# Optimization experiments

Measured on AMD Instinct MI355X. Metric: run time of the kernel, lower is better.

## Reference

```python
import jax, jax.numpy as jnp
import numpy as np

EPS_IN = 1e-5   # InstanceNorm1d eps
EPS_DM = 1e-8   # demodulation eps


def _dcoef(weight, style):
    # rsqrt(sum_i (W[o,i]*s[b,i])^2 + eps) -> [B, out]
    return jax.lax.rsqrt(jnp.einsum('oi,bi->bo', jnp.square(weight), jnp.square(style)) + EPS_DM)


def setup_inputs() -> dict:
    key = jax.random.key(0)
    ks = jax.random.split(key, 7)
    B, S, H = 8, 1024, 1024
    lim = 1.0 / np.sqrt(H)
    u = lambda k, shp: jax.random.uniform(k, shp, jnp.float32, -lim, lim)
    return {
        'x': jax.random.normal(ks[0], (B, S, H), jnp.float32),
        'q_weight': u(ks[1], (H, H)),
        'k_weight': u(ks[2], (H, H)),
        'v_weight': u(ks[3], (H, H)),
        'w_weight': u(ks[4], (H, H)),
        'u_weight': u(ks[5], (H, H)),
        'styles': jax.random.normal(ks[6], (B, 2 * H), jnp.float32) * 0.5 + 1.0,
        'num_heads': 16,
    }


def reference(x, q_weight, k_weight, v_weight, w_weight, u_weight, styles, num_heads):
    B, S, H = x.shape
    nh = num_heads
    d = H // nh
    scale = jnp.asarray(d, x.dtype) ** -0.5

    s1 = styles[:, :H]   # modulates input hidden dim of q/k/v
    s2 = styles[:, H:]   # modulates input hidden dim of w/u and v output

    # per-sample modulation + InstanceNorm over hidden dim
    x = x * s1[:, None, :]
    mu = jnp.mean(x, axis=-1, keepdims=True)
    var = jnp.mean(jnp.square(x - mu), axis=-1, keepdims=True)
    x = (x - mu) * jax.lax.rsqrt(var + EPS_IN)

    q_dc = _dcoef(q_weight, s1)  # [B,H]
    k_dc = _dcoef(k_weight, s1)
    v_dc = _dcoef(v_weight, s1)
    w_dc = _dcoef(w_weight, s2)
    u_dc = _dcoef(u_weight, s2)

    def heads(t):  # [B,S,H] -> [B,nh,S,d]
        return t.reshape(B, S, nh, d).transpose(0, 2, 1, 3)

    q = heads(jnp.einsum('bsh,oh->bso', x, q_weight) * q_dc[:, None, :])
    k = heads(jnp.einsum('bsh,oh->bso', x, k_weight) * k_dc[:, None, :])
    v_flat = jnp.einsum('bsh,oh->bso', x, v_weight) * v_dc[:, None, :] * s2[:, None, :]
    skip = v_flat
    v = heads(v_flat)

    attn = jnp.einsum('bhqd,bhkd->bhqk', q, k) * scale
    attn = jax.nn.softmax(attn, axis=-1)
    out = jnp.einsum('bhqk,bhkd->bhqd', attn, v).transpose(0, 2, 1, 3).reshape(B, S, H)

    out = jnp.einsum('bsh,oh->bso', out, w_weight) * w_dc[:, None, :]
    skip = jnp.einsum('bsh,oh->bso', skip, u_weight) * u_dc[:, None, :]
    return out + skip
```

## Files before the change

kernel.cpp:

```cpp
#include <hip/hip_runtime.h>
#include <hip/hip_bf16.h>

#define B_ 8
#define S_ 1024
#define H_ 1024
#define NH 16
#define DH 64
#define BS (B_*S_)
#define L2E 1.44269504f

typedef unsigned short u16;
typedef __attribute__((ext_vector_type(8))) short bf16x8;
typedef __attribute__((ext_vector_type(4))) float f32x4;
typedef __attribute__((ext_vector_type(4))) u16 u16x4;

#define MFMA(a,b,c) __builtin_amdgcn_mfma_f32_16x16x32_bf16((a),(b),(c),0,0,0)

__device__ __forceinline__ u16 f2bf(float f) {
  union { float f; unsigned u; } v; v.f = f;
  unsigned r = v.u + 0x7fffu + ((v.u >> 16) & 1u);
  return (u16)(r >> 16);
}

__device__ __forceinline__ unsigned packbf2(float a, float b) {
  union { __hip_bfloat162 h; unsigned u; } v;
  v.h = __float22bfloat162_rn(float2{a, b});
  return v.u;
}

__device__ __forceinline__ void gload16(const u16* g, u16* l) {
  __builtin_amdgcn_global_load_lds(
      (const __attribute__((address_space(1))) unsigned int*)g,
      (__attribute__((address_space(3))) unsigned int*)l, 16, 0, 0);
}

__global__ __launch_bounds__(256) void dcoef_kernel(
    const float* __restrict__ qw, const float* __restrict__ kw,
    const float* __restrict__ vw, const float* __restrict__ ww,
    const float* __restrict__ uw, const float* __restrict__ styles,
    float* __restrict__ dc) {
  int bi = blockIdx.x;
  int wsel = bi >> 10;
  int o = bi & 1023;
  const float* W = (wsel == 0) ? qw : (wsel == 1) ? kw : (wsel == 2) ? vw
                   : (wsel == 3) ? ww : uw;
  int soff = (wsel < 3) ? 0 : H_;
  int tid = threadIdx.x;
  float4 w4 = *(const float4*)(W + (size_t)o * H_ + tid * 4);
  float w2x = w4.x * w4.x, w2y = w4.y * w4.y, w2z = w4.z * w4.z, w2w = w4.w * w4.w;
  float acc[8];
#pragma unroll
  for (int b = 0; b < 8; b++) {
    float4 s4 = *(const float4*)(styles + (size_t)b * 2 * H_ + soff + tid * 4);
    acc[b] = w2x * s4.x * s4.x + w2y * s4.y * s4.y + w2z * s4.z * s4.z + w2w * s4.w * s4.w;
  }
#pragma unroll
  for (int off = 1; off < 64; off <<= 1)
#pragma unroll
    for (int b = 0; b < 8; b++) acc[b] += __shfl_xor(acc[b], off);
  __shared__ float red[4][8];
  int w = tid >> 6, l = tid & 63;
  if (l == 0)
#pragma unroll
    for (int b = 0; b < 8; b++) red[w][b] = acc[b];
  __syncthreads();
  if (tid < 8) {
    int b = tid;
    float v = red[0][b] + red[1][b] + red[2][b] + red[3][b];
    float r = rsqrtf(v + 1e-8f);
    if (wsel == 2) r *= styles[(size_t)b * 2 * H_ + H_ + o];
    dc[(size_t)wsel * B_ * H_ + b * H_ + o] = r;
  }
}

__global__ __launch_bounds__(256) void wconv_kernel(
    const float* __restrict__ qw, const float* __restrict__ kw,
    const float* __restrict__ vw, const float* __restrict__ ww,
    const float* __restrict__ uw, u16* __restrict__ w16) {
  int i = blockIdx.x * 256 + threadIdx.x;
  int idx = i * 4;
  int wsel = idx >> 20;
  int off = idx & (H_ * H_ - 1);
  const float* W = (wsel == 0) ? qw : (wsel == 1) ? kw : (wsel == 2) ? vw
                   : (wsel == 3) ? ww : uw;
  float4 v = *(const float4*)(W + off);
  u16x4 o = { f2bf(v.x), f2bf(v.y), f2bf(v.z), f2bf(v.w) };
  *(u16x4*)(w16 + idx) = o;
}

__global__ __launch_bounds__(256) void ln_kernel(
    const float* __restrict__ x, const float* __restrict__ styles,
    u16* __restrict__ xn) {
  int row = blockIdx.x;
  int b = row >> 10;
  int tid = threadIdx.x;
  const float4 xv = *(const float4*)(x + (size_t)row * H_ + tid * 4);
  const float4 sv = *(const float4*)(styles + (size_t)b * 2 * H_ + tid * 4);
  float v0 = xv.x * sv.x, v1 = xv.y * sv.y, v2 = xv.z * sv.z, v3 = xv.w * sv.w;
  float sum = v0 + v1 + v2 + v3;
  float sq = v0 * v0 + v1 * v1 + v2 * v2 + v3 * v3;
#pragma unroll
  for (int off = 1; off < 64; off <<= 1) {
    sum += __shfl_xor(sum, off);
    sq += __shfl_xor(sq, off);
  }
  __shared__ float rsum[4], rsq[4];
  int w = tid >> 6;
  if ((tid & 63) == 0) { rsum[w] = sum; rsq[w] = sq; }
  __syncthreads();
  sum = rsum[0] + rsum[1] + rsum[2] + rsum[3];
  sq = rsq[0] + rsq[1] + rsq[2] + rsq[3];
  float mean = sum * (1.f / H_);
  float var = sq * (1.f / H_) - mean * mean;
  float rstd = rsqrtf(var + 1e-5f);
  u16x4 o = { f2bf((v0 - mean) * rstd), f2bf((v1 - mean) * rstd),
              f2bf((v2 - mean) * rstd), f2bf((v3 - mean) * rstd) };
  *(u16x4*)(xn + (size_t)row * H_ + tid * 4) = o;
}

__device__ __forceinline__ void gemm128_core(
    const u16* __restrict__ Arow, const u16* __restrict__ Brow, int K,
    u16* ldsA, u16* ldsB, f32x4 acc[4][4]) {
  const int tid = threadIdx.x;
  const int l = tid & 63, w = tid >> 6;
  const int wm = (w >> 1) * 64, wn = (w & 1) * 64;
  const int lrow = l & 15, lko = (l >> 4) * 8;
  const int srow = tid >> 2;
  const int scol = (tid & 3) * 8;
  for (int k0 = 0; k0 < K; k0 += 32) {
    __syncthreads();
    gload16(Arow + (size_t)srow * K + k0 + scol,        ldsA + srow * 32 + scol);
    gload16(Arow + (size_t)(srow + 64) * K + k0 + scol, ldsA + (srow + 64) * 32 + scol);
    gload16(Brow + (size_t)srow * K + k0 + scol,        ldsB + srow * 32 + scol);
    gload16(Brow + (size_t)(srow + 64) * K + k0 + scol, ldsB + (srow + 64) * 32 + scol);
    __syncthreads();
    bf16x8 af[4], bfr[4];
#pragma unroll
    for (int i = 0; i < 4; i++)
      af[i] = *(const bf16x8*)&ldsA[(wm + i * 16 + lrow) * 32 + lko];
#pragma unroll
    for (int i = 0; i < 4; i++)
      bfr[i] = *(const bf16x8*)&ldsB[(wn + i * 16 + lrow) * 32 + lko];
#pragma unroll
    for (int mi = 0; mi < 4; mi++)
#pragma unroll
      for (int ni = 0; ni < 4; ni++)
        acc[mi][ni] = MFMA(af[mi], bfr[ni], acc[mi][ni]);
  }
}

__global__ __launch_bounds__(256) void qkv_kernel(
    const u16* __restrict__ xn, const u16* __restrict__ w16,
    const float* __restrict__ dc, u16* __restrict__ Qb, u16* __restrict__ Kb,
    u16* __restrict__ VT, u16* __restrict__ vfl) {
  __shared__ u16 ldsA[128 * 32], ldsB[128 * 32];
  int bm = blockIdx.x;
  int bn = blockIdx.y;
  f32x4 acc[4][4] = {};
  gemm128_core(xn + (size_t)bm * 128 * H_, w16 + (size_t)bn * 128 * H_, H_,
               ldsA, ldsB, acc);
  int l = threadIdx.x & 63, w = threadIdx.x >> 6;
  int wm = (w >> 1) * 64, wn = (w & 1) * 64;
  int wsel = bn >> 3;
  int col0 = (bn & 7) * 128 + wn;
  int row0 = bm * 128 + wm;
  const float* dcw = dc + (size_t)wsel * B_ * H_;
  float extra = (wsel == 0) ? 0.125f * L2E : 1.0f;
#pragma unroll
  for (int mi = 0; mi < 4; mi++) {
#pragma unroll
    for (int ni = 0; ni < 4; ni++) {
      int col = col0 + ni * 16 + (l & 15);
      int hh = col >> 6, dd = col & 63;
      int s_base = (row0 + mi * 16 + (l >> 4) * 4) & 1023;
      int b = (row0 + mi * 16 + (l >> 4) * 4) >> 10;
      float dcv = dcw[b * H_ + col] * extra;
      u16 bv[4];
#pragma unroll
      for (int rr = 0; rr < 4; rr++)
        bv[rr] = f2bf(acc[mi][ni][rr] * dcv);
      if (wsel == 0) {
#pragma unroll
        for (int rr = 0; rr < 4; rr++)
          Qb[((size_t)(b * NH + hh) * S_ + s_base + rr) * DH + dd] = bv[rr];
      } else if (wsel == 1) {
#pragma unroll
        for (int rr = 0; rr < 4; rr++)
          Kb[((size_t)(b * NH + hh) * S_ + s_base + rr) * DH + dd] = bv[rr];
      } else {
        u16x4 pv = { bv[0], bv[1], bv[2], bv[3] };
        *(u16x4*)&VT[((size_t)(b * NH + hh) * DH + dd) * S_ + s_base] = pv;
#pragma unroll
        for (int rr = 0; rr < 4; rr++)
          vfl[(size_t)(row0 + mi * 16 + (l >> 4) * 4 + rr) * H_ + col] = bv[rr];
      }
    }
  }
}

__global__ __launch_bounds__(512) void attn_kernel(
    const u16* __restrict__ Qb, const u16* __restrict__ Kb,
    const u16* __restrict__ VT, u16* __restrict__ xat) {
  __shared__ u16 ldsK[2][64 * 64];
  __shared__ u16 ldsV[2][64 * 64];
  __shared__ unsigned pls_all[8][16 * 36];
  int tid = threadIdx.x;
  int l = tid & 63, w = tid >> 6;
  int qblk = blockIdx.x;
  int h = blockIdx.y;
  int b = blockIdx.z;
  int q0 = qblk * 256 + w * 32;
  const u16* Qp = Qb + ((size_t)(b * NH + h) * S_ + q0) * DH;
  const u16* Kp = Kb + (size_t)(b * NH + h) * S_ * DH;
  const u16* Vp = VT + (size_t)(b * NH + h) * DH * S_;
  unsigned* pls = pls_all[w];
  int lr = l & 15, lg = l >> 4;
  int sw = (lr & 7) << 3;
  bf16x8 qfA0 = *(const bf16x8*)(Qp + lr * 64 + lg * 8);
  bf16x8 qfA1 = *(const bf16x8*)(Qp + lr * 64 + 32 + lg * 8);
  bf16x8 qfB0 = *(const bf16x8*)(Qp + (16 + lr) * 64 + lg * 8);
  bf16x8 qfB1 = *(const bf16x8*)(Qp + (16 + lr) * 64 + 32 + lg * 8);
  int srow = tid >> 3, schunk = tid & 7;
  int ssw = (schunk * 8) ^ ((srow & 7) << 3);
  const u16* Ksrc = Kp + (size_t)srow * DH + ssw;
  const u16* Vsrc = Vp + (size_t)srow * S_ + ssw;
  u16* Kdst = &ldsK[0][srow * 64 + schunk * 8];
  u16* Vdst = &ldsV[0][srow * 64 + schunk * 8];
  gload16(Ksrc, Kdst);
  gload16(Vsrc, Vdst);
  f32x4 accA[4] = {}, accB[4] = {};
  float mA = -1e30f, lsA = 0.f, mB = -1e30f, lsB = 0.f;
  asm volatile("s_waitcnt vmcnt(0)" ::: "memory");
  __builtin_amdgcn_s_barrier();
  int cur = 0;
  for (int t = 0; t < 16; ++t) {
    if (t < 15) {
      gload16(Ksrc + (size_t)(t + 1) * 64 * DH, Kdst + (cur ^ 1) * 64 * 64);
      gload16(Vsrc + (size_t)(t + 1) * 64,      Vdst + (cur ^ 1) * 64 * 64);
    }
    const u16* Kt = &ldsK[cur][0];
    const u16* Vt = &ldsV[cur][0];
#pragma unroll
    for (int g = 0; g < 2; g++) {
      bf16x8 q0f = (g == 0) ? qfA0 : qfB0;
      bf16x8 q1f = (g == 0) ? qfA1 : qfB1;
      float mreg = (g == 0) ? mA : mB;
      float lsreg = (g == 0) ? lsA : lsB;
      f32x4 st[4];
#pragma unroll
      for (int nt = 0; nt < 4; nt++) {
        bf16x8 kf0 = *(const bf16x8*)&Kt[(nt * 16 + lr) * 64 + ((lg * 8) ^ sw)];
        bf16x8 kf1 = *(const bf16x8*)&Kt[(nt * 16 + lr) * 64 + ((32 + lg * 8) ^ sw)];
        f32x4 z = {0.f, 0.f, 0.f, 0.f};
        z = MFMA(kf0, q0f, z);
        z = MFMA(kf1, q1f, z);
        st[nt] = z;
      }
      float tm = st[0][0];
#pragma unroll
      for (int nt = 0; nt < 4; nt++)
#pragma unroll
        for (int rr = 0; rr < 4; rr++) tm = fmaxf(tm, st[nt][rr]);
      tm = fmaxf(tm, __shfl_xor(tm, 16));
      tm = fmaxf(tm, __shfl_xor(tm, 32));
      float mn = fmaxf(mreg, tm);
      float al = __builtin_exp2f(mreg - mn);
      float rs = 0.f;
#pragma unroll
      for (int nt = 0; nt < 4; nt++)
#pragma unroll
        for (int rr = 0; rr < 4; rr++) {
          st[nt][rr] = __builtin_exp2f(st[nt][rr] - mn);
          rs += st[nt][rr];
        }
      rs += __shfl_xor(rs, 16);
      rs += __shfl_xor(rs, 32);
      if (g == 0) { mA = mn; lsA = lsA * al + rs; }
      else        { mB = mn; lsB = lsB * al + rs; }
      {
        unsigned* base = pls + lr * 36;
#pragma unroll
        for (int nt = 0; nt < 4; nt++) {
          uint2 pw = { packbf2(st[nt][0], st[nt][1]),
                       packbf2(st[nt][2], st[nt][3]) };
          *(uint2*)&base[nt * 8 + lg * 2] = pw;
        }
      }
      bf16x8 pb0 = *(const bf16x8*)&pls[lr * 36 + lg * 4];
      bf16x8 pb1 = *(const bf16x8*)&pls[lr * 36 + 16 + lg * 4];
#pragma unroll
      for (int nt = 0; nt < 4; nt++) {
        bf16x8 vf0 = *(const bf16x8*)&Vt[(nt * 16 + lr) * 64 + ((lg * 8) ^ sw)];
        bf16x8 vf1 = *(const bf16x8*)&Vt[(nt * 16 + lr) * 64 + ((32 + lg * 8) ^ sw)];
        if (g == 0) {
          accA[nt][0] *= al; accA[nt][1] *= al; accA[nt][2] *= al; accA[nt][3] *= al;
          accA[nt] = MFMA(vf0, pb0, accA[nt]);
          accA[nt] = MFMA(vf1, pb1, accA[nt]);
        } else {
          accB[nt][0] *= al; accB[nt][1] *= al; accB[nt][2] *= al; accB[nt][3] *= al;
          accB[nt] = MFMA(vf0, pb0, accB[nt]);
          accB[nt] = MFMA(vf1, pb1, accB[nt]);
        }
      }
    }
    asm volatile("s_waitcnt vmcnt(0)" ::: "memory");
    __builtin_amdgcn_s_barrier();
    cur ^= 1;
  }
  float invA = 1.f / lsA, invB = 1.f / lsB;
#pragma unroll
  for (int nt = 0; nt < 4; nt++) {
    u16x4 oA = { f2bf(accA[nt][0] * invA), f2bf(accA[nt][1] * invA),
                 f2bf(accA[nt][2] * invA), f2bf(accA[nt][3] * invA) };
    *(u16x4*)(xat + ((size_t)(b * S_) + q0 + lr) * H_ + h * DH + nt * 16 + lg * 4) = oA;
    u16x4 oB = { f2bf(accB[nt][0] * invB), f2bf(accB[nt][1] * invB),
                 f2bf(accB[nt][2] * invB), f2bf(accB[nt][3] * invB) };
    *(u16x4*)(xat + ((size_t)(b * S_) + q0 + 16 + lr) * H_ + h * DH + nt * 16 + lg * 4) = oB;
  }
}

__global__ __launch_bounds__(256) void out_kernel(
    const u16* __restrict__ xat, const u16* __restrict__ vfl,
    const u16* __restrict__ w16, const float* __restrict__ dc,
    float* __restrict__ out) {
  __shared__ u16 ldsA[128 * 32], ldsB[128 * 32];
  int bm = blockIdx.x;
  int bn = blockIdx.y;
  f32x4 acc[4][4] = {};
  gemm128_core(xat + (size_t)bm * 128 * H_,
               w16 + (size_t)3 * H_ * H_ + (size_t)bn * 128 * H_, H_,
               ldsA, ldsB, acc);
  int l = threadIdx.x & 63, w = threadIdx.x >> 6;
  int wm = (w >> 1) * 64, wn = (w & 1) * 64;
  int col0 = bn * 128 + wn;
  int row0 = bm * 128 + wm;
  int b = row0 >> 10;
  const float* wdc = dc + (size_t)3 * B_ * H_ + b * H_;
  const float* udc = dc + (size_t)4 * B_ * H_ + b * H_;
  float ratio[4], ud[4];
#pragma unroll
  for (int ni = 0; ni < 4; ni++) {
    int col = col0 + ni * 16 + (l & 15);
    ud[ni] = udc[col];
    ratio[ni] = wdc[col] / ud[ni];
  }
#pragma unroll
  for (int mi = 0; mi < 4; mi++)
#pragma unroll
    for (int ni = 0; ni < 4; ni++)
#pragma unroll
      for (int rr = 0; rr < 4; rr++) acc[mi][ni][rr] *= ratio[ni];
  gemm128_core(vfl + (size_t)bm * 128 * H_,
               w16 + (size_t)4 * H_ * H_ + (size_t)bn * 128 * H_, H_,
               ldsA, ldsB, acc);
#pragma unroll
  for (int mi = 0; mi < 4; mi++)
#pragma unroll
    for (int ni = 0; ni < 4; ni++) {
      int col = col0 + ni * 16 + (l & 15);
#pragma unroll
      for (int rr = 0; rr < 4; rr++) {
        int row = row0 + mi * 16 + (l >> 4) * 4 + rr;
        out[(size_t)row * H_ + col] = acc[mi][ni][rr] * ud[ni];
      }
    }
}

extern "C" void kernel_launch(void* const* d_in, const int* in_sizes, int n_in,
                              void* d_out, int out_size, void* d_ws, size_t ws_size,
                              hipStream_t stream) {
  const float* x = (const float*)d_in[0];
  const float* qw = (const float*)d_in[1];
  const float* kw = (const float*)d_in[2];
  const float* vw = (const float*)d_in[3];
  const float* ww = (const float*)d_in[4];
  const float* uw = (const float*)d_in[5];
  const float* styles = (const float*)d_in[6];
  float* out = (float*)d_out;

  char* ws = (char*)d_ws;
  size_t need = 163840 + (size_t)5 * H_ * H_ * 2 + (size_t)6 * BS * H_ * 2;
  if (ws_size < need) return;
  float* dc = (float*)ws;
  u16* w16 = (u16*)(ws + 163840);
  u16* xn  = w16 + (size_t)5 * H_ * H_;
  u16* Qb  = xn + (size_t)BS * H_;
  u16* Kb  = Qb + (size_t)BS * H_;
  u16* VT  = Kb + (size_t)BS * H_;
  u16* vfl = VT + (size_t)BS * H_;
  u16* xat = vfl + (size_t)BS * H_;

  dcoef_kernel<<<dim3(5 * H_), dim3(256), 0, stream>>>(qw, kw, vw, ww, uw, styles, dc);
  wconv_kernel<<<dim3(5120), dim3(256), 0, stream>>>(qw, kw, vw, ww, uw, w16);
  ln_kernel<<<dim3(BS), dim3(256), 0, stream>>>(x, styles, xn);
  qkv_kernel<<<dim3(64, 24), dim3(256), 0, stream>>>(xn, w16, dc, Qb, Kb, VT, vfl);
  attn_kernel<<<dim3(4, NH, B_), dim3(512), 0, stream>>>(Qb, Kb, VT, xat);
  out_kernel<<<dim3(64, 8), dim3(256), 0, stream>>>(xat, vfl, w16, dc, out);
}
```

Baseline: 228.7 us.

## Triple-buffer attention K/V loads, add lazy softmax rescale, setprio, and remap blocks

The attention kernel moves from double-buffered to triple-buffered K/V tiles in LDS, prefetching two tiles ahead and waiting with vmcnt(2) so global loads overlap more compute. Online-softmax rescaling is skipped when the new tile max stays within a threshold of the running max (a lazy-rescale trick that stays exact). MFMA sections are wrapped in s_setprio, and the grid is flattened with an index remap that spreads heads and batches across XCDs for better L2 locality. The extra LDS buffer may reduce occupancy.

```diff
diff --git a/kernel.cpp b/kernel.cpp
--- a/kernel.cpp
+++ b/kernel.cpp
@@ -201,14 +201,16 @@
 __global__ __launch_bounds__(512) void attn_kernel(
     const u16* __restrict__ Qb, const u16* __restrict__ Kb,
     const u16* __restrict__ VT, u16* __restrict__ xat) {
-  __shared__ u16 ldsK[2][64 * 64];
-  __shared__ u16 ldsV[2][64 * 64];
+  __shared__ u16 ldsK[3][64 * 64];
+  __shared__ u16 ldsV[3][64 * 64];
   __shared__ unsigned pls_all[8][16 * 36];
   int tid = threadIdx.x;
   int l = tid & 63, w = tid >> 6;
-  int qblk = blockIdx.x;
-  int h = blockIdx.y;
-  int b = blockIdx.z;
+  int id = blockIdx.x;
+  int r = id & 7, rest = id >> 3;
+  int qblk = rest & 3, a = rest >> 2;
+  int hl = a * 8 + r;
+  int h = hl & 15, b = hl >> 4;
   int q0 = qblk * 256 + w * 32;
   const u16* Qp = Qb + ((size_t)(b * NH + h) * S_ + q0) * DH;
   const u16* Kp = Kb + (size_t)(b * NH + h) * S_ * DH;
@@ -216,27 +218,29 @@
   unsigned* pls = pls_all[w];
   int lr = l & 15, lg = l >> 4;
   int sw = (lr & 7) << 3;
+  int srow = tid >> 3, schunk = tid & 7;
+  int ssw = (schunk * 8) ^ ((srow & 7) << 3);
+  const u16* Ksrc = Kp + (size_t)srow * DH + ssw;
+  const u16* Vsrc = Vp + (size_t)srow * S_ + ssw;
+  int sdst = srow * 64 + schunk * 8;
+  gload16(Ksrc, &ldsK[0][sdst]);
+  gload16(Vsrc, &ldsV[0][sdst]);
+  gload16(Ksrc + 64 * DH, &ldsK[1][sdst]);
+  gload16(Vsrc + 64,      &ldsV[1][sdst]);
   bf16x8 qfA0 = *(const bf16x8*)(Qp + lr * 64 + lg * 8);
   bf16x8 qfA1 = *(const bf16x8*)(Qp + lr * 64 + 32 + lg * 8);
   bf16x8 qfB0 = *(const bf16x8*)(Qp + (16 + lr) * 64 + lg * 8);
   bf16x8 qfB1 = *(const bf16x8*)(Qp + (16 + lr) * 64 + 32 + lg * 8);
-  int srow = tid >> 3, schunk = tid & 7;
-  int ssw = (schunk * 8) ^ ((srow & 7) << 3);
-  const u16* Ksrc = Kp + (size_t)srow * DH + ssw;
-  const u16* Vsrc = Vp + (size_t)srow * S_ + ssw;
-  u16* Kdst = &ldsK[0][srow * 64 + schunk * 8];
-  u16* Vdst = &ldsV[0][srow * 64 + schunk * 8];
-  gload16(Ksrc, Kdst);
-  gload16(Vsrc, Vdst);
   f32x4 accA[4] = {}, accB[4] = {};
   float mA = -1e30f, lsA = 0.f, mB = -1e30f, lsB = 0.f;
-  asm volatile("s_waitcnt vmcnt(0)" ::: "memory");
+  asm volatile("s_waitcnt vmcnt(2)" ::: "memory");
   __builtin_amdgcn_s_barrier();
   int cur = 0;
   for (int t = 0; t < 16; ++t) {
-    if (t < 15) {
-      gload16(Ksrc + (size_t)(t + 1) * 64 * DH, Kdst + (cur ^ 1) * 64 * 64);
-      gload16(Vsrc + (size_t)(t + 1) * 64,      Vdst + (cur ^ 1) * 64 * 64);
+    if (t + 2 < 16) {
+      int nb = cur + 2; if (nb >= 3) nb -= 3;
+      gload16(Ksrc + (size_t)(t + 2) * 64 * DH, &ldsK[nb][sdst]);
+      gload16(Vsrc + (size_t)(t + 2) * 64,      &ldsV[nb][sdst]);
     }
     const u16* Kt = &ldsK[cur][0];
     const u16* Vt = &ldsV[cur][0];
@@ -245,8 +249,8 @@
       bf16x8 q0f = (g == 0) ? qfA0 : qfB0;
       bf16x8 q1f = (g == 0) ? qfA1 : qfB1;
       float mreg = (g == 0) ? mA : mB;
-      float lsreg = (g == 0) ? lsA : lsB;
       f32x4 st[4];
+      __builtin_amdgcn_s_setprio(1);
 #pragma unroll
       for (int nt = 0; nt < 4; nt++) {
         bf16x8 kf0 = *(const bf16x8*)&Kt[(nt * 16 + lr) * 64 + ((lg * 8) ^ sw)];
@@ -256,6 +260,7 @@
         z = MFMA(kf1, q1f, z);
         st[nt] = z;
       }
+      __builtin_amdgcn_s_setprio(0);
       float tm = st[0][0];
 #pragma unroll
       for (int nt = 0; nt < 4; nt++)
@@ -263,8 +268,9 @@
         for (int rr = 0; rr < 4; rr++) tm = fmaxf(tm, st[nt][rr]);
       tm = fmaxf(tm, __shfl_xor(tm, 16));
       tm = fmaxf(tm, __shfl_xor(tm, 32));
-      float mn = fmaxf(mreg, tm);
-      float al = __builtin_exp2f(mreg - mn);
+      bool noresc = (__all(tm <= mreg + 8.f) != 0);
+      float mn = noresc ? mreg : fmaxf(mreg, tm);
+      float al = noresc ? 1.f : __builtin_exp2f(mreg - mn);
       float rs = 0.f;
 #pragma unroll
       for (int nt = 0; nt < 4; nt++)
@@ -286,26 +292,40 @@
           *(uint2*)&base[nt * 8 + lg * 2] = pw;
         }
       }
+      if (!noresc) {
+#pragma unroll
+        for (int nt = 0; nt < 4; nt++) {
+          if (g == 0) {
+            accA[nt][0] *= al; accA[nt][1] *= al; accA[nt][2] *= al; accA[nt][3] *= al;
+          } else {
+            accB[nt][0] *= al; accB[nt][1] *= al; accB[nt][2] *= al; accB[nt][3] *= al;
+          }
+        }
+      }
       bf16x8 pb0 = *(const bf16x8*)&pls[lr * 36 + lg * 4];
       bf16x8 pb1 = *(const bf16x8*)&pls[lr * 36 + 16 + lg * 4];
+      __builtin_amdgcn_s_setprio(1);
 #pragma unroll
       for (int nt = 0; nt < 4; nt++) {
         bf16x8 vf0 = *(const bf16x8*)&Vt[(nt * 16 + lr) * 64 + ((lg * 8) ^ sw)];
         bf16x8 vf1 = *(const bf16x8*)&Vt[(nt * 16 + lr) * 64 + ((32 + lg * 8) ^ sw)];
         if (g == 0) {
-          accA[nt][0] *= al; accA[nt][1] *= al; accA[nt][2] *= al; accA[nt][3] *= al;
           accA[nt] = MFMA(vf0, pb0, accA[nt]);
           accA[nt] = MFMA(vf1, pb1, accA[nt]);
         } else {
-          accB[nt][0] *= al; accB[nt][1] *= al; accB[nt][2] *= al; accB[nt][3] *= al;
           accB[nt] = MFMA(vf0, pb0, accB[nt]);
           accB[nt] = MFMA(vf1, pb1, accB[nt]);
         }
       }
+      __builtin_amdgcn_s_setprio(0);
     }
-    asm volatile("s_waitcnt vmcnt(0)" ::: "memory");
-    __builtin_amdgcn_s_barrier();
-    cur ^= 1;
+    if (t < 14) {
+      asm volatile("s_waitcnt vmcnt(2)" ::: "memory");
+    } else if (t == 14) {
+      asm volatile("s_waitcnt vmcnt(0)" ::: "memory");
+    }
+    if (t < 15) __builtin_amdgcn_s_barrier();
+    cur = (cur == 2) ? 0 : cur + 1;
   }
   float invA = 1.f / lsA, invB = 1.f / lsB;
 #pragma unroll
@@ -394,6 +414,6 @@
   wconv_kernel<<<dim3(5120), dim3(256), 0, stream>>>(qw, kw, vw, ww, uw, w16);
   ln_kernel<<<dim3(BS), dim3(256), 0, stream>>>(x, styles, xn);
   qkv_kernel<<<dim3(64, 24), dim3(256), 0, stream>>>(xn, w16, dc, Qb, Kb, VT, vfl);
-  attn_kernel<<<dim3(4, NH, B_), dim3(512), 0, stream>>>(Qb, Kb, VT, xat);
+  attn_kernel<<<dim3(512), dim3(512), 0, stream>>>(Qb, Kb, VT, xat);
   out_kernel<<<dim3(64, 8), dim3(256), 0, stream>>>(xat, vfl, w16, dc, out);
 }
```

New measurement: 217.3 us. 1.05x faster.
